# Kernel tuning notes

Hardware: AMD Instinct MI355X
Metric: run time of the kernel (lower is better)

## Reference

```python
import jax, jax.numpy as jnp
import numpy as np

N = 50000      # nodes
E = 800000     # edges
H = 4          # heads (all layers)
D = 64         # per-head out dim (n_hidden == n_classes == 64)
IN = 256       # in_feats; also H*D so identity residual is valid
NEG_SLOPE = 0.2


def setup_inputs() -> dict:
    key = jax.random.key(0)
    ks = jax.random.split(key, 16)
    x = jax.random.normal(ks[0], (N, IN), dtype=jnp.float32)
    src = jax.random.randint(ks[1], (E,), 0, N, dtype=jnp.int32)
    dst = jax.random.randint(ks[2], (E,), 0, N, dtype=jnp.int32)
    inp = {"x": x, "src": src, "dst": dst}
    fan_ins = [IN, H * D, H * D]  # layer input widths
    for i, fin in enumerate(fan_ins):
        s = 1.0 / np.sqrt(fin)
        inp[f"W{i}"] = jax.random.normal(ks[3 + 4 * i], (fin, H * D), dtype=jnp.float32) * s
        inp[f"al{i}"] = jax.random.normal(ks[4 + 4 * i], (H, D), dtype=jnp.float32) * s
        inp[f"ar{i}"] = jax.random.normal(ks[5 + 4 * i], (H, D), dtype=jnp.float32) * s
        inp[f"b{i}"] = jnp.zeros((H * D,), dtype=jnp.float32)
    return inp


def _gat_layer(h, src, dst, W, al, ar, b, residual, activate):
    # project: [N, in] @ [in, H*D] -> [N, H, D]
    feat = (h @ W).reshape(-1, H, D)
    el = jnp.sum(feat * al, axis=-1)            # [N, H]
    er = jnp.sum(feat * ar, axis=-1)            # [N, H]
    e = jax.nn.leaky_relu(el[src] + er[dst], NEG_SLOPE)  # [E, H]
    # edge softmax per destination node (stable: subtract per-dst max)
    emax = jax.ops.segment_max(e, dst, num_segments=N)  # [N, H]
    e = jnp.exp(e - emax[dst])
    denom = jax.ops.segment_sum(e, dst, num_segments=N)  # [N, H]
    alpha = e / denom[dst]                               # [E, H]
    # message + scatter-aggregate: [E, H, D] summed into [N, H, D]
    out = jax.ops.segment_sum(alpha[:, :, None] * feat[src], dst, num_segments=N)
    if residual:
        out = out + h.reshape(-1, H, D)  # identity residual (in == H*D)
    out = out + b.reshape(1, H, D)
    if activate:
        out = jax.nn.elu(out)
    return out


def reference(x, src, dst, W0, al0, ar0, b0, W1, al1, ar1, b1, W2, al2, ar2, b2):
    h = _gat_layer(x, src, dst, W0, al0, ar0, b0, False, True).reshape(N, H * D)
    h = _gat_layer(h, src, dst, W1, al1, ar1, b1, True, True).reshape(N, H * D)
    h = _gat_layer(h, src, dst, W2, al2, ar2, b2, True, False).mean(axis=1)  # [N, D]
    return h
```

## Files before the change

kernel.cpp:

```cpp
#include <hip/hip_runtime.h>
#include <math.h>

#define N_NODES 50000
#define N_EDGES 800000
#define HD 256
#define NHEAD 4
#define DH 64

typedef short bf16x8 __attribute__((ext_vector_type(8)));
typedef float f32x4 __attribute__((ext_vector_type(4)));

__device__ __forceinline__ unsigned short f2bf(float f) {
    unsigned u = __float_as_uint(f);
    return (unsigned short)((u + 0x7fffu + ((u >> 16) & 1u)) >> 16);
}
__device__ __forceinline__ float bf2f(unsigned short h) {
    return __uint_as_float((unsigned)h << 16);
}
__device__ __forceinline__ int origk(int k) {
    return (k & ~63) | ((k & 3) * 16 + ((k >> 2) & 15));
}

__global__ void packw_k(const float* __restrict__ W0, const float* __restrict__ W1,
                        const float* __restrict__ W2, unsigned short* __restrict__ Wp) {
    int blk = blockIdx.x;
    int L = blk >> 7, t = blk & 127;
    const float* W = L == 0 ? W0 : L == 1 ? W1 : W2;
    int nt = t >> 3, kt = t & 7;
    int lane = threadIdx.x;
    int col = nt * 16 + (lane & 15);
    int kb = kt * 32 + (lane >> 4) * 8;
    unsigned short v[8];
#pragma unroll
    for (int j = 0; j < 8; j++) {
        int k = kb + j;
        if (L > 0) k = origk(k);
        v[j] = f2bf(W[(size_t)k * 256 + col]);
    }
    *(bf16x8*)(Wp + ((size_t)(L * 128 + t) * 64 + lane) * 8) = *(bf16x8*)v;
}

template <bool AFP32>
__global__ __launch_bounds__(256) void gemm_k(const void* __restrict__ Av,
                                              const unsigned short* __restrict__ Wp,
                                              const float* __restrict__ al,
                                              const float* __restrict__ ar,
                                              unsigned short* __restrict__ C,
                                              float* __restrict__ el,
                                              float* __restrict__ er, int M) {
    __shared__ unsigned short Asl[64 * 256];
    int tid = threadIdx.x, wv = tid >> 6, lane = tid & 63;
    int bm = blockIdx.x * 64;
    if (AFP32) {
        const float* A = (const float*)Av;
#pragma unroll
        for (int i = 0; i < 8; i++) {
            int chunk = i * 256 + tid;
            int r = chunk >> 5, kc = (chunk & 31) * 8;
            float4 f0, f1;
            if (bm + r < M) {
                const float* p = A + (size_t)(bm + r) * 256 + kc;
                f0 = *(const float4*)p;
                f1 = *(const float4*)(p + 4);
            } else {
                f0 = f1 = make_float4(0.f, 0.f, 0.f, 0.f);
            }
            unsigned short tmp[8] = {f2bf(f0.x), f2bf(f0.y), f2bf(f0.z), f2bf(f0.w),
                                     f2bf(f1.x), f2bf(f1.y), f2bf(f1.z), f2bf(f1.w)};
            int b = (r * 512 + kc * 2) ^ ((r & 7) << 4);
            *(bf16x8*)((char*)Asl + b) = *(bf16x8*)tmp;
        }
    } else {
        const unsigned short* A = (const unsigned short*)Av;
#pragma unroll
        for (int i = 0; i < 8; i++) {
            int chunk = i * 256 + wv * 64 + lane;
            int r = chunk >> 5;
            int c16 = (chunk & 31) ^ (r & 7);
            const unsigned short* src = A + (size_t)(bm + r) * 256 + c16 * 8;
            __builtin_amdgcn_global_load_lds(
                (const __attribute__((address_space(1))) unsigned int*)src,
                (__attribute__((address_space(3))) unsigned int*)
                    ((char*)Asl + (size_t)(i * 256 + wv * 64) * 16),
                16, 0, 0);
        }
    }
    __syncthreads();
    f32x4 acc[4][4] = {};
    const unsigned short* wbase = Wp + (size_t)(wv * 4) * 8 * 64 * 8;
#pragma unroll
    for (int kk = 0; kk < 8; kk++) {
        bf16x8 a[4], b[4];
#pragma unroll
        for (int m = 0; m < 4; m++) {
            int r = m * 16 + (lane & 15);
            int kb = kk * 32 + (lane >> 4) * 8;
            int byt = (r * 512 + kb * 2) ^ ((r & 7) << 4);
            a[m] = *(const bf16x8*)((const char*)Asl + byt);
        }
#pragma unroll
        for (int n = 0; n < 4; n++)
            b[n] = *(const bf16x8*)(wbase + ((size_t)(n * 8 + kk) * 64 + lane) * 8);
#pragma unroll
        for (int m = 0; m < 4; m++)
#pragma unroll
            for (int n = 0; n < 4; n++)
                acc[m][n] = __builtin_amdgcn_mfma_f32_16x16x32_bf16(a[m], b[n],
                                                                    acc[m][n], 0, 0, 0);
    }
    int rr = lane >> 4, cc = lane & 15;
    float alv[4], arv[4];
#pragma unroll
    for (int n = 0; n < 4; n++) {
        alv[n] = al[wv * 64 + n * 16 + cc];
        arv[n] = ar[wv * 64 + n * 16 + cc];
    }
    float vl[16], vr[16];
#pragma unroll
    for (int m = 0; m < 4; m++)
#pragma unroll
        for (int r = 0; r < 4; r++) {
            float ep = 0.f, rp = 0.f;
#pragma unroll
            for (int n = 0; n < 4; n++) {
                ep = fmaf(acc[m][n][r], alv[n], ep);
                rp = fmaf(acc[m][n][r], arv[n], rp);
            }
            vl[m * 4 + r] = ep;
            vr[m * 4 + r] = rp;
        }
    float l8[8], r8[8];
#pragma unroll
    for (int i = 0; i < 8; i++) {
        float xs = (cc & 1) ? vl[2 * i] : vl[2 * i + 1];
        float xk = (cc & 1) ? vl[2 * i + 1] : vl[2 * i];
        l8[i] = xk + __shfl_xor(xs, 1);
        float ys = (cc & 1) ? vr[2 * i] : vr[2 * i + 1];
        float yk = (cc & 1) ? vr[2 * i + 1] : vr[2 * i];
        r8[i] = yk + __shfl_xor(ys, 1);
    }
    float l4[4], r4[4];
#pragma unroll
    for (int i = 0; i < 4; i++) {
        float xs = (cc & 2) ? l8[2 * i] : l8[2 * i + 1];
        float xk = (cc & 2) ? l8[2 * i + 1] : l8[2 * i];
        l4[i] = xk + __shfl_xor(xs, 2);
        float ys = (cc & 2) ? r8[2 * i] : r8[2 * i + 1];
        float yk = (cc & 2) ? r8[2 * i + 1] : r8[2 * i];
        r4[i] = yk + __shfl_xor(ys, 2);
    }
    float l2[2], r2[2];
#pragma unroll
    for (int i = 0; i < 2; i++) {
        float xs = (cc & 4) ? l4[2 * i] : l4[2 * i + 1];
        float xk = (cc & 4) ? l4[2 * i + 1] : l4[2 * i];
        l2[i] = xk + __shfl_xor(xs, 4);
        float ys = (cc & 4) ? r4[2 * i] : r4[2 * i + 1];
        float yk = (cc & 4) ? r4[2 * i + 1] : r4[2 * i];
        r2[i] = yk + __shfl_xor(ys, 4);
    }
    {
        float xs = (cc & 8) ? l2[0] : l2[1];
        float xk = (cc & 8) ? l2[1] : l2[0];
        float lv = xk + __shfl_xor(xs, 8);
        float ys = (cc & 8) ? r2[0] : r2[1];
        float yk = (cc & 8) ? r2[1] : r2[0];
        float rv = yk + __shfl_xor(ys, 8);
        int row_e = bm + (cc >> 2) * 16 + rr * 4 + (cc & 3);
        if (row_e < M) {
            el[(size_t)row_e * NHEAD + wv] = lv;
            er[(size_t)row_e * NHEAD + wv] = rv;
        }
    }
#pragma unroll
    for (int m = 0; m < 4; m++) {
#pragma unroll
        for (int r = 0; r < 4; r++) {
            int row = bm + m * 16 + rr * 4 + r;
            if (row < M) {
                unsigned short p4[4] = {f2bf(acc[m][0][r]), f2bf(acc[m][1][r]),
                                        f2bf(acc[m][2][r]), f2bf(acc[m][3][r])};
                *(ushort4*)(C + (size_t)row * 256 + wv * 64 + cc * 4) = *(ushort4*)p4;
            }
        }
    }
}

__global__ void hist_k(const int* __restrict__ dst, int* __restrict__ deg) {
    int e = blockIdx.x * 256 + threadIdx.x;
    if (e < N_EDGES) atomicAdd(&deg[dst[e]], 1);
}

__global__ __launch_bounds__(1024) void scan1_k(const int* __restrict__ deg,
                                                int* __restrict__ rowptr,
                                                int* __restrict__ bsum) {
    __shared__ int wsum[16];
    int tid = threadIdx.x, lane = tid & 63, wv = tid >> 6;
    int i = blockIdx.x * 1024 + tid;
    int v = (i < N_NODES) ? deg[i] : 0;
    int sc = v;
#pragma unroll
    for (int o = 1; o < 64; o <<= 1) {
        int t = __shfl_up(sc, o);
        if (lane >= o) sc += t;
    }
    if (lane == 63) wsum[wv] = sc;
    __syncthreads();
    if (wv == 0 && lane < 16) {
        int ws = wsum[lane];
#pragma unroll
        for (int o = 1; o < 16; o <<= 1) {
            int t = __shfl_up(ws, o);
            if (lane >= o) ws += t;
        }
        wsum[lane] = ws;
    }
    __syncthreads();
    int incl = sc + (wv > 0 ? wsum[wv - 1] : 0);
    if (i < N_NODES) rowptr[i + 1] = incl;
    if (tid == 1023) bsum[blockIdx.x] = incl;
}

__global__ __launch_bounds__(1024) void scan3_k(int* __restrict__ rowptr,
                                                const int* __restrict__ bsum,
                                                int* __restrict__ cursor, int nb) {
    __shared__ int boff_s;
    int tid = threadIdx.x;
    if (tid < 64) {
        int v = (tid < nb) ? bsum[tid] : 0;
        int sc = v;
#pragma unroll
        for (int o = 1; o < 64; o <<= 1) {
            int t = __shfl_up(sc, o);
            if ((tid & 63) >= o) sc += t;
        }
        if (tid == (int)blockIdx.x) boff_s = sc - v;
    }
    __syncthreads();
    int off = boff_s;
    int i = blockIdx.x * 1024 + tid;
    if (blockIdx.x == 0 && tid == 0) { rowptr[0] = 0; cursor[0] = 0; }
    if (i < N_NODES) {
        int v = rowptr[i + 1] + off;
        rowptr[i + 1] = v;
        if (i + 1 < N_NODES) cursor[i + 1] = v;
    }
}

__global__ void scatter_k(const int* __restrict__ src, const int* __restrict__ dst,
                          int* __restrict__ cursor, int* __restrict__ csr_src) {
    int e = blockIdx.x * 256 + threadIdx.x;
    if (e >= N_EDGES) return;
    int pos = atomicAdd(&cursor[dst[e]], 1);
    csr_src[pos] = src[e];
}

template <int MODE>
__global__ __launch_bounds__(256) void agg_k(const int* __restrict__ rowptr,
                                             const int* __restrict__ csr_src,
                                             const float* __restrict__ el,
                                             const float* __restrict__ er,
                                             const unsigned short* __restrict__ feat,
                                             const unsigned short* __restrict__ resid,
                                             const float* __restrict__ bias,
                                             float* __restrict__ out,
                                             unsigned short* __restrict__ hb) {
    __shared__ int   ws_s[4][64];
    __shared__ float ws_w[4][4][68];
    int wv = threadIdx.x >> 6, lane = threadIdx.x & 63;
    int node = blockIdx.x * 4 + wv;
    if (node >= N_NODES) return;
    int beg = rowptr[node], end = rowptr[node + 1];
    float4 er4 = *(const float4*)(er + (size_t)node * 4);
    float4 acc0 = make_float4(0.f, 0.f, 0.f, 0.f);
    float4 acc1 = make_float4(0.f, 0.f, 0.f, 0.f);
    float4 den = make_float4(0.f, 0.f, 0.f, 0.f);
    int h = lane >> 4;
    int l8 = lane * 8;
    const char* fb = (const char*)feat;
    for (int base = beg; base < end; base += 64) {
        int j = base + lane;
        int soff = 0;
        float4 w = make_float4(0.f, 0.f, 0.f, 0.f);
        if (j < end) {
            int s = csr_src[j];
            soff = s << 9;
            float4 l4 = *(const float4*)(el + (size_t)s * 4);
            float vx = l4.x + er4.x; vx = vx > 0.f ? vx : 0.2f * vx;
            float vy = l4.y + er4.y; vy = vy > 0.f ? vy : 0.2f * vy;
            float vz = l4.z + er4.z; vz = vz > 0.f ? vz : 0.2f * vz;
            float vw = l4.w + er4.w; vw = vw > 0.f ? vw : 0.2f * vw;
            w.x = expf(vx); w.y = expf(vy); w.z = expf(vz); w.w = expf(vw);
            den.x += w.x; den.y += w.y; den.z += w.z; den.w += w.w;
        }
        ws_s[wv][lane] = soff;
        ws_w[wv][0][lane] = w.x;
        ws_w[wv][1][lane] = w.y;
        ws_w[wv][2][lane] = w.z;
        ws_w[wv][3][lane] = w.w;
        __builtin_amdgcn_wave_barrier();
        int cnt = end - base; if (cnt > 64) cnt = 64;
        int cnt4 = (cnt + 3) & ~3;
        for (int k = 0; k < cnt4; k += 4) {
            int4   so = *(const int4*)&ws_s[wv][k];
            float4 w4 = *(const float4*)&ws_w[wv][h][k];
            ushort4 u0 = *(const ushort4*)(fb + (so.x + l8));
            ushort4 u1 = *(const ushort4*)(fb + (so.y + l8));
            ushort4 u2 = *(const ushort4*)(fb + (so.z + l8));
            ushort4 u3 = *(const ushort4*)(fb + (so.w + l8));
            acc0.x = fmaf(w4.x, bf2f(u0.x), acc0.x);
            acc0.y = fmaf(w4.x, bf2f(u0.y), acc0.y);
            acc0.z = fmaf(w4.x, bf2f(u0.z), acc0.z);
            acc0.w = fmaf(w4.x, bf2f(u0.w), acc0.w);
            acc1.x = fmaf(w4.y, bf2f(u1.x), acc1.x);
            acc1.y = fmaf(w4.y, bf2f(u1.y), acc1.y);
            acc1.z = fmaf(w4.y, bf2f(u1.z), acc1.z);
            acc1.w = fmaf(w4.y, bf2f(u1.w), acc1.w);
            acc0.x = fmaf(w4.z, bf2f(u2.x), acc0.x);
            acc0.y = fmaf(w4.z, bf2f(u2.y), acc0.y);
            acc0.z = fmaf(w4.z, bf2f(u2.z), acc0.z);
            acc0.w = fmaf(w4.z, bf2f(u2.w), acc0.w);
            acc1.x = fmaf(w4.w, bf2f(u3.x), acc1.x);
            acc1.y = fmaf(w4.w, bf2f(u3.y), acc1.y);
            acc1.z = fmaf(w4.w, bf2f(u3.z), acc1.z);
            acc1.w = fmaf(w4.w, bf2f(u3.w), acc1.w);
        }
        __builtin_amdgcn_wave_barrier();
    }
    float4 acc;
    acc.x = acc0.x + acc1.x; acc.y = acc0.y + acc1.y;
    acc.z = acc0.z + acc1.z; acc.w = acc0.w + acc1.w;
#pragma unroll
    for (int o = 1; o < 64; o <<= 1) {
        den.x += __shfl_xor(den.x, o);
        den.y += __shfl_xor(den.y, o);
        den.z += __shfl_xor(den.z, o);
        den.w += __shfl_xor(den.w, o);
    }
    float den_me = h == 0 ? den.x : h == 1 ? den.y : h == 2 ? den.z : den.w;
    float r = den_me > 0.f ? 1.f / den_me : 0.f;
    int cc = lane & 15;
    float4 b4;
    b4.x = bias[h * 64 + 0 * 16 + cc];
    b4.y = bias[h * 64 + 1 * 16 + cc];
    b4.z = bias[h * 64 + 2 * 16 + cc];
    b4.w = bias[h * 64 + 3 * 16 + cc];
    float4 o4;
    o4.x = acc.x * r + b4.x;
    o4.y = acc.y * r + b4.y;
    o4.z = acc.z * r + b4.z;
    o4.w = acc.w * r + b4.w;
    if (MODE >= 1) {
        ushort4 r4 = *(const ushort4*)(resid + (size_t)node * HD + lane * 4);
        o4.x += bf2f(r4.x); o4.y += bf2f(r4.y);
        o4.z += bf2f(r4.z); o4.w += bf2f(r4.w);
    }
    if (MODE <= 1) {
        o4.x = o4.x > 0.f ? o4.x : expm1f(o4.x);
        o4.y = o4.y > 0.f ? o4.y : expm1f(o4.y);
        o4.z = o4.z > 0.f ? o4.z : expm1f(o4.z);
        o4.w = o4.w > 0.f ? o4.w : expm1f(o4.w);
        ushort4 hv;
        hv.x = f2bf(o4.x); hv.y = f2bf(o4.y); hv.z = f2bf(o4.z); hv.w = f2bf(o4.w);
        *(ushort4*)(hb + (size_t)node * HD + lane * 4) = hv;
    } else {
        o4.x += __shfl_xor(o4.x, 16); o4.x += __shfl_xor(o4.x, 32);
        o4.y += __shfl_xor(o4.y, 16); o4.y += __shfl_xor(o4.y, 32);
        o4.z += __shfl_xor(o4.z, 16); o4.z += __shfl_xor(o4.z, 32);
        o4.w += __shfl_xor(o4.w, 16); o4.w += __shfl_xor(o4.w, 32);
        if (lane < 16) {
            float* po = out + (size_t)node * DH;
            po[0 * 16 + lane] = o4.x * 0.25f;
            po[1 * 16 + lane] = o4.y * 0.25f;
            po[2 * 16 + lane] = o4.z * 0.25f;
            po[3 * 16 + lane] = o4.w * 0.25f;
        }
    }
}

extern "C" void kernel_launch(void* const* d_in, const int* in_sizes, int n_in,
                              void* d_out, int out_size, void* d_ws, size_t ws_size,
                              hipStream_t stream) {
    const float* x   = (const float*)d_in[0];
    const int*   src = (const int*)d_in[1];
    const int*   dst = (const int*)d_in[2];
    const float* W[3]  = {(const float*)d_in[3], (const float*)d_in[7],  (const float*)d_in[11]};
    const float* al[3] = {(const float*)d_in[4], (const float*)d_in[8],  (const float*)d_in[12]};
    const float* ar[3] = {(const float*)d_in[5], (const float*)d_in[9],  (const float*)d_in[13]};
    const float* bb[3] = {(const float*)d_in[6], (const float*)d_in[10], (const float*)d_in[14]};

    size_t big = (size_t)N_NODES * HD;
    unsigned short* featb = (unsigned short*)d_ws;
    unsigned short* hb1 = featb + big;
    unsigned short* hb2 = hb1 + big;
    float* el = (float*)(hb2 + big);
    float* er = el + (size_t)N_NODES * NHEAD;
    int* deg     = (int*)(er + (size_t)N_NODES * NHEAD);
    int* rowptr  = deg + 50048;
    int* cursor  = rowptr + 50048;
    int* csr_src = cursor + 50048;
    int* bsum    = csr_src + N_EDGES;
    unsigned short* Wp = (unsigned short*)(bsum + 64);

    const int NB = (N_NODES + 1023) / 1024;

    packw_k<<<384, 64, 0, stream>>>(W[0], W[1], W[2], Wp);
    hipMemsetAsync(deg, 0, (size_t)N_NODES * 4, stream);
    hist_k<<<N_EDGES / 256, 256, 0, stream>>>(dst, deg);
    scan1_k<<<NB, 1024, 0, stream>>>(deg, rowptr, bsum);
    scan3_k<<<NB, 1024, 0, stream>>>(rowptr, bsum, cursor, NB);
    scatter_k<<<N_EDGES / 256, 256, 0, stream>>>(src, dst, cursor, csr_src);

    int ggrid = (N_NODES + 63) / 64;
    int agrid = (N_NODES + 3) / 4;

    gemm_k<true><<<ggrid, 256, 0, stream>>>(x, Wp, al[0], ar[0], featb, el, er, N_NODES);
    agg_k<0><<<agrid, 256, 0, stream>>>(rowptr, csr_src, el, er, featb,
                                        nullptr, bb[0], nullptr, hb1);
    gemm_k<false><<<ggrid, 256, 0, stream>>>(hb1, Wp + (size_t)1 * 128 * 64 * 8,
                                             al[1], ar[1], featb, el, er, N_NODES);
    agg_k<1><<<agrid, 256, 0, stream>>>(rowptr, csr_src, el, er, featb,
                                        hb1, bb[1], nullptr, hb2);
    gemm_k<false><<<ggrid, 256, 0, stream>>>(hb2, Wp + (size_t)2 * 128 * 64 * 8,
                                             al[2], ar[2], featb, el, er, N_NODES);
    agg_k<2><<<agrid, 256, 0, stream>>>(rowptr, csr_src, el, er, featb,
                                        hb2, bb[2], (float*)d_out, nullptr);
}
```

Baseline: 350.9 us.

## Double-buffer bf16 GEMM tiles, fold deg memset into packw, vectorize CSR build

The bf16-input GEMM now handles two 64-row tiles per block. Both tiles' loads are issued up front via global_load_lds, so the second tile's load overlaps the first tile's MFMA work (partial vmcnt wait). The separate deg memset is folded into the weight-packing kernel, and the histogram and scatter kernels each process two edges per thread with int2 loads. This trades higher LDS use per block (halving occupancy headroom) for fewer launches and overlapped load latency.

```diff
diff --git a/kernel.cpp b/kernel.cpp
--- a/kernel.cpp
+++ b/kernel.cpp
@@ -22,12 +22,14 @@
 }
 
 __global__ void packw_k(const float* __restrict__ W0, const float* __restrict__ W1,
-                        const float* __restrict__ W2, unsigned short* __restrict__ Wp) {
+                        const float* __restrict__ W2, unsigned short* __restrict__ Wp,
+                        int* __restrict__ deg) {
     int blk = blockIdx.x;
     int L = blk >> 7, t = blk & 127;
     const float* W = L == 0 ? W0 : L == 1 ? W1 : W2;
     int nt = t >> 3, kt = t & 7;
     int lane = threadIdx.x;
+    for (int i = blk * 64 + lane; i < N_NODES; i += 384 * 64) deg[i] = 0;
     int col = nt * 16 + (lane & 15);
     int kb = kt * 32 + (lane >> 4) * 8;
     unsigned short v[8];
@@ -40,74 +42,37 @@
     *(bf16x8*)(Wp + ((size_t)(L * 128 + t) * 64 + lane) * 8) = *(bf16x8*)v;
 }
 
-template <bool AFP32>
-__global__ __launch_bounds__(256) void gemm_k(const void* __restrict__ Av,
-                                              const unsigned short* __restrict__ Wp,
+__device__ __forceinline__ void mfma_tile(const unsigned short* Asl,
+                                          const unsigned short* wbase,
+                                          int lane, f32x4 acc[4][4]) {
+#pragma unroll
+    for (int kk = 0; kk < 8; kk++) {
+        bf16x8 a[4], b[4];
+#pragma unroll
+        for (int m = 0; m < 4; m++) {
+            int r = m * 16 + (lane & 15);
+            int kb = kk * 32 + (lane >> 4) * 8;
+            int byt = (r * 512 + kb * 2) ^ ((r & 7) << 4);
+            a[m] = *(const bf16x8*)((const char*)Asl + byt);
+        }
+#pragma unroll
+        for (int n = 0; n < 4; n++)
+            b[n] = *(const bf16x8*)(wbase + ((size_t)(n * 8 + kk) * 64 + lane) * 8);
+#pragma unroll
+        for (int m = 0; m < 4; m++)
+#pragma unroll
+            for (int n = 0; n < 4; n++)
+                acc[m][n] = __builtin_amdgcn_mfma_f32_16x16x32_bf16(a[m], b[n],
+                                                                    acc[m][n], 0, 0, 0);
+    }
+}
+
+__device__ __forceinline__ void epilogue_tile(f32x4 acc[4][4], int bm, int wv, int lane,
                                               const float* __restrict__ al,
                                               const float* __restrict__ ar,
                                               unsigned short* __restrict__ C,
                                               float* __restrict__ el,
                                               float* __restrict__ er, int M) {
-    __shared__ unsigned short Asl[64 * 256];
-    int tid = threadIdx.x, wv = tid >> 6, lane = tid & 63;
-    int bm = blockIdx.x * 64;
-    if (AFP32) {
-        const float* A = (const float*)Av;
-#pragma unroll
-        for (int i = 0; i < 8; i++) {
-            int chunk = i * 256 + tid;
-            int r = chunk >> 5, kc = (chunk & 31) * 8;
-            float4 f0, f1;
-            if (bm + r < M) {
-                const float* p = A + (size_t)(bm + r) * 256 + kc;
-                f0 = *(const float4*)p;
-                f1 = *(const float4*)(p + 4);
-            } else {
-                f0 = f1 = make_float4(0.f, 0.f, 0.f, 0.f);
-            }
-            unsigned short tmp[8] = {f2bf(f0.x), f2bf(f0.y), f2bf(f0.z), f2bf(f0.w),
-                                     f2bf(f1.x), f2bf(f1.y), f2bf(f1.z), f2bf(f1.w)};
-            int b = (r * 512 + kc * 2) ^ ((r & 7) << 4);
-            *(bf16x8*)((char*)Asl + b) = *(bf16x8*)tmp;
-        }
-    } else {
-        const unsigned short* A = (const unsigned short*)Av;
-#pragma unroll
-        for (int i = 0; i < 8; i++) {
-            int chunk = i * 256 + wv * 64 + lane;
-            int r = chunk >> 5;
-            int c16 = (chunk & 31) ^ (r & 7);
-            const unsigned short* src = A + (size_t)(bm + r) * 256 + c16 * 8;
-            __builtin_amdgcn_global_load_lds(
-                (const __attribute__((address_space(1))) unsigned int*)src,
-                (__attribute__((address_space(3))) unsigned int*)
-                    ((char*)Asl + (size_t)(i * 256 + wv * 64) * 16),
-                16, 0, 0);
-        }
-    }
-    __syncthreads();
-    f32x4 acc[4][4] = {};
-    const unsigned short* wbase = Wp + (size_t)(wv * 4) * 8 * 64 * 8;
-#pragma unroll
-    for (int kk = 0; kk < 8; kk++) {
-        bf16x8 a[4], b[4];
-#pragma unroll
-        for (int m = 0; m < 4; m++) {
-            int r = m * 16 + (lane & 15);
-            int kb = kk * 32 + (lane >> 4) * 8;
-            int byt = (r * 512 + kb * 2) ^ ((r & 7) << 4);
-            a[m] = *(const bf16x8*)((const char*)Asl + byt);
-        }
-#pragma unroll
-        for (int n = 0; n < 4; n++)
-            b[n] = *(const bf16x8*)(wbase + ((size_t)(n * 8 + kk) * 64 + lane) * 8);
-#pragma unroll
-        for (int m = 0; m < 4; m++)
-#pragma unroll
-            for (int n = 0; n < 4; n++)
-                acc[m][n] = __builtin_amdgcn_mfma_f32_16x16x32_bf16(a[m], b[n],
-                                                                    acc[m][n], 0, 0, 0);
-    }
     int rr = lane >> 4, cc = lane & 15;
     float alv[4], arv[4];
 #pragma unroll
@@ -186,9 +151,100 @@
     }
 }
 
+__global__ __launch_bounds__(256) void gemm0_k(const float* __restrict__ A,
+                                               const unsigned short* __restrict__ Wp,
+                                               const float* __restrict__ al,
+                                               const float* __restrict__ ar,
+                                               unsigned short* __restrict__ C,
+                                               float* __restrict__ el,
+                                               float* __restrict__ er, int M) {
+    __shared__ unsigned short Asl[64 * 256];
+    int tid = threadIdx.x, wv = tid >> 6, lane = tid & 63;
+    int bm = blockIdx.x * 64;
+#pragma unroll
+    for (int i = 0; i < 8; i++) {
+        int chunk = i * 256 + tid;
+        int r = chunk >> 5, kc = (chunk & 31) * 8;
+        float4 f0, f1;
+        if (bm + r < M) {
+            const float* p = A + (size_t)(bm + r) * 256 + kc;
+            f0 = *(const float4*)p;
+            f1 = *(const float4*)(p + 4);
+        } else {
+            f0 = f1 = make_float4(0.f, 0.f, 0.f, 0.f);
+        }
+        unsigned short tmp[8] = {f2bf(f0.x), f2bf(f0.y), f2bf(f0.z), f2bf(f0.w),
+                                 f2bf(f1.x), f2bf(f1.y), f2bf(f1.z), f2bf(f1.w)};
+        int b = (r * 512 + kc * 2) ^ ((r & 7) << 4);
+        *(bf16x8*)((char*)Asl + b) = *(bf16x8*)tmp;
+    }
+    __syncthreads();
+    const unsigned short* wbase = Wp + (size_t)(wv * 4) * 8 * 64 * 8;
+    f32x4 acc[4][4] = {};
+    mfma_tile(Asl, wbase, lane, acc);
+    epilogue_tile(acc, bm, wv, lane, al, ar, C, el, er, M);
+}
+
+__global__ __launch_bounds__(256) void gemm2_k(const unsigned short* __restrict__ A,
+                                               const unsigned short* __restrict__ Wp,
+                                               const float* __restrict__ al,
+                                               const float* __restrict__ ar,
+                                               unsigned short* __restrict__ C,
+                                               float* __restrict__ el,
+                                               float* __restrict__ er, int M) {
+    __shared__ unsigned short Asl[2][64 * 256];
+    int tid = threadIdx.x, wv = tid >> 6, lane = tid & 63;
+    int bm0 = blockIdx.x * 128, bm1 = bm0 + 64;
+#pragma unroll
+    for (int i = 0; i < 8; i++) {
+        int chunk = i * 256 + tid;
+        int r = chunk >> 5;
+        int c16 = (chunk & 31) ^ (r & 7);
+        int grow = bm0 + r; if (grow >= M) grow = M - 1;
+        __builtin_amdgcn_global_load_lds(
+            (const __attribute__((address_space(1))) unsigned int*)
+                (A + (size_t)grow * 256 + c16 * 8),
+            (__attribute__((address_space(3))) unsigned int*)
+                ((char*)Asl[0] + (size_t)chunk * 16),
+            16, 0, 0);
+    }
+#pragma unroll
+    for (int i = 0; i < 8; i++) {
+        int chunk = i * 256 + tid;
+        int r = chunk >> 5;
+        int c16 = (chunk & 31) ^ (r & 7);
+        int grow = bm1 + r; if (grow >= M) grow = M - 1;
+        __builtin_amdgcn_global_load_lds(
+            (const __attribute__((address_space(1))) unsigned int*)
+                (A + (size_t)grow * 256 + c16 * 8),
+            (__attribute__((address_space(3))) unsigned int*)
+                ((char*)Asl[1] + (size_t)chunk * 16),
+            16, 0, 0);
+    }
+    asm volatile("s_waitcnt vmcnt(8)" ::: "memory");
+    __builtin_amdgcn_sched_barrier(0);
+    __builtin_amdgcn_s_barrier();
+    const unsigned short* wbase = Wp + (size_t)(wv * 4) * 8 * 64 * 8;
+    f32x4 acc[4][4] = {};
+    mfma_tile(Asl[0], wbase, lane, acc);
+    asm volatile("s_waitcnt vmcnt(0)" ::: "memory");
+    __builtin_amdgcn_sched_barrier(0);
+    __builtin_amdgcn_s_barrier();
+    epilogue_tile(acc, bm0, wv, lane, al, ar, C, el, er, M);
+    f32x4 acc2[4][4] = {};
+    mfma_tile(Asl[1], wbase, lane, acc2);
+    epilogue_tile(acc2, bm1, wv, lane, al, ar, C, el, er, M);
+}
+
 __global__ void hist_k(const int* __restrict__ dst, int* __restrict__ deg) {
-    int e = blockIdx.x * 256 + threadIdx.x;
-    if (e < N_EDGES) atomicAdd(&deg[dst[e]], 1);
+    int e = (blockIdx.x * 256 + threadIdx.x) * 2;
+    if (e + 1 < N_EDGES) {
+        int2 d2 = *(const int2*)(dst + e);
+        atomicAdd(&deg[d2.x], 1);
+        atomicAdd(&deg[d2.y], 1);
+    } else if (e < N_EDGES) {
+        atomicAdd(&deg[dst[e]], 1);
+    }
 }
 
 __global__ __launch_bounds__(1024) void scan1_k(const int* __restrict__ deg,
@@ -249,10 +305,15 @@
 
 __global__ void scatter_k(const int* __restrict__ src, const int* __restrict__ dst,
                           int* __restrict__ cursor, int* __restrict__ csr_src) {
-    int e = blockIdx.x * 256 + threadIdx.x;
-    if (e >= N_EDGES) return;
-    int pos = atomicAdd(&cursor[dst[e]], 1);
-    csr_src[pos] = src[e];
+    int e = (blockIdx.x * 256 + threadIdx.x) * 2;
+    if (e + 1 < N_EDGES) {
+        int2 s2 = *(const int2*)(src + e);
+        int2 d2 = *(const int2*)(dst + e);
+        csr_src[atomicAdd(&cursor[d2.x], 1)] = s2.x;
+        csr_src[atomicAdd(&cursor[d2.y], 1)] = s2.y;
+    } else if (e < N_EDGES) {
+        csr_src[atomicAdd(&cursor[dst[e]], 1)] = src[e];
+    }
 }
 
 template <int MODE>
@@ -404,25 +465,25 @@
 
     const int NB = (N_NODES + 1023) / 1024;
 
-    packw_k<<<384, 64, 0, stream>>>(W[0], W[1], W[2], Wp);
-    hipMemsetAsync(deg, 0, (size_t)N_NODES * 4, stream);
-    hist_k<<<N_EDGES / 256, 256, 0, stream>>>(dst, deg);
+    packw_k<<<384, 64, 0, stream>>>(W[0], W[1], W[2], Wp, deg);
+    hist_k<<<(N_EDGES / 2 + 255) / 256, 256, 0, stream>>>(dst, deg);
     scan1_k<<<NB, 1024, 0, stream>>>(deg, rowptr, bsum);
     scan3_k<<<NB, 1024, 0, stream>>>(rowptr, bsum, cursor, NB);
-    scatter_k<<<N_EDGES / 256, 256, 0, stream>>>(src, dst, cursor, csr_src);
-
-    int ggrid = (N_NODES + 63) / 64;
+    scatter_k<<<(N_EDGES / 2 + 255) / 256, 256, 0, stream>>>(src, dst, cursor, csr_src);
+
+    int g0grid = (N_NODES + 63) / 64;
+    int g2grid = (N_NODES + 127) / 128;
     int agrid = (N_NODES + 3) / 4;
 
-    gemm_k<true><<<ggrid, 256, 0, stream>>>(x, Wp, al[0], ar[0], featb, el, er, N_NODES);
+    gemm0_k<<<g0grid, 256, 0, stream>>>(x, Wp, al[0], ar[0], featb, el, er, N_NODES);
     agg_k<0><<<agrid, 256, 0, stream>>>(rowptr, csr_src, el, er, featb,
                                         nullptr, bb[0], nullptr, hb1);
-    gemm_k<false><<<ggrid, 256, 0, stream>>>(hb1, Wp + (size_t)1 * 128 * 64 * 8,
-                                             al[1], ar[1], featb, el, er, N_NODES);
+    gemm2_k<<<g2grid, 256, 0, stream>>>(hb1, Wp + (size_t)1 * 128 * 64 * 8,
+                                        al[1], ar[1], featb, el, er, N_NODES);
     agg_k<1><<<agrid, 256, 0, stream>>>(rowptr, csr_src, el, er, featb,
                                         hb1, bb[1], nullptr, hb2);
-    gemm_k<false><<<ggrid, 256, 0, stream>>>(hb2, Wp + (size_t)2 * 128 * 64 * 8,
-                                             al[2], ar[2], featb, el, er, N_NODES);
+    gemm2_k<<<g2grid, 256, 0, stream>>>(hb2, Wp + (size_t)2 * 128 * 64 * 8,
+                                        al[2], ar[2], featb, el, er, N_NODES);
     agg_k<2><<<agrid, 256, 0, stream>>>(rowptr, csr_src, el, er, featb,
                                         hb2, bb[2], (float*)d_out, nullptr);
 }
```

After: 340.0 us. 1.03x faster.
